# Kernel optimization log

Measured on AMD Instinct MI355X. Metric: run time of the kernel, lower is better.

## Reference

```python
import jax, jax.numpy as jnp
from jax import lax
import numpy as np

EPS = 1e-6
LN_EPS = 1e-3
B, T, F = 8, 2048, 80
STRIDE, NFILT = 2, 64
FEAT_P = 20              # ceil(80 / 4) after two stride-2 convs
CAPS_IN_N, CAPS_IN_D = 32, 8
CAPS_COV_N, CAPS_COV_D = 32, 8
CLASS_N, CAPS_CLS_D = 31, 8
WINDOW, LPAD, RPAD = 3, 1, 1
N_ITER = 3


def conv2d(x, w, b, stride):
    y = lax.conv_general_dilated(x, w, (stride, stride), 'SAME',
                                 dimension_numbers=('NHWC', 'HWIO', 'NHWC'))
    return y + b


def feat_mask(x, lengths, factor):
    # zero out time steps >= ceil(len/factor)
    S = x.shape[1]
    vl = jnp.ceil(lengths.astype(jnp.float32) / factor).astype(jnp.int32)
    m = (jnp.arange(S)[None, :] < vl[:, None]).astype(x.dtype)
    return x * m.reshape(m.shape + (1,) * (x.ndim - 2))


def squash(x, axis=-1):
    sq = jnp.sum(x * x, axis=axis, keepdims=True)
    return x * (sq / (1.0 + sq) / jnp.sqrt(sq + EPS))


def layernorm(x):
    mu = jnp.mean(x, -1, keepdims=True)
    var = jnp.var(x, -1, keepdims=True)
    return (x - mu) / jnp.sqrt(var + LN_EPS)


def window_concat(x):
    # [B,S,N,D] -> [B,S,N*WINDOW,D] (windowed context gather)
    S = x.shape[1]
    xp = jnp.pad(x, ((0, 0), (LPAD, RPAD), (0, 0), (0, 0)))
    return jnp.concatenate([xp[:, j:j + S] for j in range(WINDOW)], axis=2)


def dynamic_routing(u_hat, logit_mask):
    # u_hat: [B,S,I,O,D] -> v: [B,S,O,D]
    b0 = jnp.zeros(u_hat.shape[:4], u_hat.dtype)

    def body(b, _):
        c = jax.nn.softmax(b + logit_mask, axis=3)          # coupling coeffs
        s = jnp.einsum('bsio,bsiod->bsod', c, u_hat)
        v = squash(s, -1)
        b = b + jnp.einsum('bsiod,bsod->bsio', u_hat, v)    # agreement update
        return b, v

    _, vs = lax.scan(body, b0, None, length=N_ITER)
    return vs[-1]


def _forward(inputs, conv0_w1, conv0_b1, conv0_w2, conv0_b2,
             conv1_w1, conv1_b1, conv1_w2, conv1_b2,
             proj_w, proj_b, enc_w1, enc_b1, enc_w2, enc_b2,
             W0, B0, W1, B1, input_lengths):
    # --- CapsulationLayer: maxout conv feature extraction ---
    x = inputs[..., None]                                    # [B,T,F,1]
    x = jnp.maximum(conv2d(x, conv0_w1, conv0_b1, STRIDE),
                    conv2d(x, conv0_w2, conv0_b2, STRIDE))
    x = feat_mask(x, input_lengths, STRIDE)                  # [B,T/2,F/2,64]
    x = jnp.maximum(conv2d(x, conv1_w1, conv1_b1, STRIDE),
                    conv2d(x, conv1_w2, conv1_b2, STRIDE))
    x = feat_mask(x, input_lengths, STRIDE ** 2)             # [B,S,20,64]
    b, S = x.shape[0], x.shape[1]

    # --- primary capsules ---
    emb = x.reshape(b, S, FEAT_P * NFILT) @ proj_w + proj_b  # [B,S,32]
    emb = emb[..., None]                                     # [B,S,32,1]
    emb = jnp.maximum(conv2d(emb, enc_w1, enc_b1, 1),
                      conv2d(emb, enc_w2, enc_b2, 1))        # [B,S,32,8]
    emb = feat_mask(emb, input_lengths, STRIDE ** 2)
    emb = squash(emb, -1)
    emb = layernorm(emb.reshape(b, S, -1)).reshape(b, S, CAPS_IN_N, CAPS_IN_D)

    # --- caps layer 0: primary(windowed) -> convolution capsules ---
    win = window_concat(emb)                                 # [B,S,96,8]
    u = jnp.einsum('iodk,bsik->bsiod', W0, win) + B0[None, None]
    v = dynamic_routing(u, jnp.zeros((1, 1, 1, CAPS_COV_N), u.dtype))
    emb = layernorm(v.reshape(b, S, -1)).reshape(b, S, CAPS_COV_N, CAPS_COV_D)

    # --- caps layer 1: conv(windowed) -> class capsules (blank masked) ---
    win = window_concat(emb)                                 # [B,S,96,8]
    u = jnp.einsum('iodk,bsik->bsiod', W1, win) + B1[None, None]
    lm = jnp.concatenate([jnp.full((1, 1, 1, 1), -1e9, u.dtype),
                          jnp.zeros((1, 1, 1, CLASS_N - 1), u.dtype)], -1)
    v = dynamic_routing(u, lm)
    v = layernorm(v.reshape(b, S, -1)).reshape(b, S, CLASS_N, CAPS_CLS_D)

    # --- class capsule lengths + output layernorm ---
    out = jnp.sqrt(jnp.sum(v * v, -1) + EPS)                 # [B,S,31]
    return layernorm(out)


def setup_inputs() -> dict:
    key = jax.random.key(0)
    ks = list(jax.random.split(key, 24))
    n = lambda i, shape, s=0.1: jax.random.normal(ks[i], shape, jnp.float32) * s
    d = {
        'inputs': jax.random.normal(ks[0], (B, T, F), jnp.float32),
        'conv0_w1': n(1, (3, 3, 1, NFILT)), 'conv0_b1': n(2, (NFILT,)),
        'conv0_w2': n(3, (3, 3, 1, NFILT)), 'conv0_b2': n(4, (NFILT,)),
        'conv1_w1': n(5, (3, 3, NFILT, NFILT), 0.05), 'conv1_b1': n(6, (NFILT,)),
        'conv1_w2': n(7, (3, 3, NFILT, NFILT), 0.05), 'conv1_b2': n(8, (NFILT,)),
        'proj_w': n(9, (FEAT_P * NFILT, CAPS_IN_N), 0.02), 'proj_b': n(10, (CAPS_IN_N,)),
        'enc_w1': n(11, (3, 3, 1, CAPS_IN_D)), 'enc_b1': n(12, (CAPS_IN_D,)),
        'enc_w2': n(13, (3, 3, 1, CAPS_IN_D)), 'enc_b2': n(14, (CAPS_IN_D,)),
        'W0': n(15, (CAPS_IN_N * WINDOW, CAPS_COV_N, CAPS_COV_D, CAPS_IN_D)),
        'B0': n(16, (CAPS_IN_N * WINDOW, CAPS_COV_N, CAPS_COV_D)),
        'W1': n(17, (CAPS_COV_N * WINDOW, CLASS_N, CAPS_CLS_D, CAPS_COV_D)),
        'B1': n(18, (CAPS_COV_N * WINDOW, CLASS_N, CAPS_CLS_D)),
        'input_lengths': jax.random.randint(ks[19], (B,), T // 2, T + 1, jnp.int32),
    }
    return d


def reference(inputs, conv0_w1, conv0_b1, conv0_w2, conv0_b2,
              conv1_w1, conv1_b1, conv1_w2, conv1_b2,
              proj_w, proj_b, enc_w1, enc_b1, enc_w2, enc_b2,
              W0, B0, W1, B1, input_lengths):
    return _forward(inputs, conv0_w1, conv0_b1, conv0_w2, conv0_b2,
                    conv1_w1, conv1_b1, conv1_w2, conv1_b2,
                    proj_w, proj_b, enc_w1, enc_b1, enc_w2, enc_b2,
                    W0, B0, W1, B1, input_lengths)
```

## Files before the change

kernel.cpp:

```cpp
#include <hip/hip_runtime.h>

typedef unsigned short u16;
typedef unsigned int u32;
typedef short short8 __attribute__((ext_vector_type(8)));
typedef float f32x4 __attribute__((ext_vector_type(4)));
typedef _Float16 h2 __attribute__((ext_vector_type(2)));
typedef __fp16 fp16v2 __attribute__((ext_vector_type(2)));

#define DEV static __device__ __forceinline__

DEV float bf2f(u16 v) { return __uint_as_float((u32)v << 16); }
DEV u16 f2bf(float f) {
    u32 x = __float_as_uint(f);
    return (u16)((x + 0x7fffu + ((x >> 16) & 1u)) >> 16);
}
DEV u16 f2h(float f) {
    union { _Float16 h; u16 u; } c; c.h = (_Float16)f; return c.u;
}
DEV u32 pack2h(float a, float b) {
#if __has_builtin(__builtin_amdgcn_cvt_pkrtz)
    union { fp16v2 h; u32 u; } c;
    c.h = __builtin_amdgcn_cvt_pkrtz(a, b);
    return c.u;
#else
    union { u32 u; _Float16 h[2]; } c;
    c.h[0] = (_Float16)a; c.h[1] = (_Float16)b; return c.u;
#endif
}
DEV h2 u2h(u32 x) { union { u32 u; h2 h; } c; c.u = x; return c.h; }
DEV u32 h2u(h2 v) { union { h2 h; u32 u; } c; c.h = v; return c.u; }

#if __has_builtin(__builtin_amdgcn_fdot2)
DEV float dot2(u32 a, u32 b, float c) {
    return __builtin_amdgcn_fdot2(u2h(a), u2h(b), c, false);
}
#else
DEV float dot2(u32 a, u32 b, float c) {
    h2 ha = u2h(a), hb = u2h(b);
    c = fmaf((float)ha[0], (float)hb[0], c);
    return fmaf((float)ha[1], (float)hb[1], c);
}
#endif

constexpr int Bn = 8, Tn = 2048, Fn = 80, NF = 64;
constexpr int H1 = 1024, W1n = 40;
constexpr int Sn = 512,  W2n = 20;
constexpr int PK = 1280;
constexpr int I0 = 96;
constexpr int O0 = 32;
constexpr int O1 = 31;
constexpr int CPW = 52;
constexpr int NW0 = I0 * O0 * 8 * 8;
constexpr int NW1 = I0 * O1 * 8 * 8;
constexpr int KC1 = 576;

template <int CTRL>
DEV float dpp_mov(float x) {
    return __int_as_float(__builtin_amdgcn_update_dpp(
        0, __float_as_int(x), CTRL, 0xF, 0xF, true));
}
template <int CTRL>
DEV u32 dppu(u32 x) {
    return (u32)__builtin_amdgcn_update_dpp(0, (int)x, CTRL, 0xF, 0xF, true);
}
DEV float sum8(float x) {
    x += dpp_mov<0xB1>(x);
    x += dpp_mov<0x4E>(x);
    x += dpp_mov<0x141>(x);
    return x;
}
DEV u32 sum8h(u32 x) {
    x = h2u(u2h(x) + u2h(dppu<0xB1>(x)));
    x = h2u(u2h(x) + u2h(dppu<0x4E>(x)));
    x = h2u(u2h(x) + u2h(dppu<0x141>(x)));
    return x;
}

DEV float2 block_sum2(float a, float b, int tid, float* lds ) {
    #pragma unroll
    for (int m = 1; m < 64; m <<= 1) {
        a += __shfl_xor(a, m);
        b += __shfl_xor(b, m);
    }
    int wid = tid >> 6;
    __syncthreads();
    if ((tid & 63) == 0) { lds[wid * 2] = a; lds[wid * 2 + 1] = b; }
    __syncthreads();
    float ra = lds[0] + lds[2] + lds[4] + lds[6];
    float rb = lds[1] + lds[3] + lds[5] + lds[7];
    return make_float2(ra, rb);
}

__global__ void __launch_bounds__(256) k_prep(
        const float* __restrict__ w0, const float* __restrict__ w1c,
        const float* __restrict__ cw1, const float* __restrict__ cb1,
        const float* __restrict__ cw2, const float* __restrict__ cb2,
        u16* __restrict__ w0h, u16* __restrict__ w1h,
        u16* __restrict__ wt, float* __restrict__ biasi) {
    int idx = blockIdx.x * 256 + threadIdx.x;
    if (idx < NW0) w0h[idx] = f2h(w0[idx]);
    if (idx < NW1) w1h[idx] = f2h(w1c[idx]);
    if (idx < 128 * KC1) {
        int n = idx / KC1, k = idx - n * KC1;
        int c = n >> 1, s = n & 1;
        const float* w = s ? cw2 : cw1;
        wt[idx] = f2bf(w[k * 64 + c]);
    }
    if (idx < 128) {
        int c = idx >> 1, s = idx & 1;
        biasi[idx] = (s ? cb2 : cb1)[c];
    }
}

__global__ void __launch_bounds__(256) k_conv0(
        const float* __restrict__ in,
        const float* __restrict__ w1, const float* __restrict__ b1,
        const float* __restrict__ w2, const float* __restrict__ b2,
        const int* __restrict__ lens, u16* __restrict__ x1) {
    __shared__ float srow[3][82];
    int blk = blockIdx.x;
    int h = blk & (H1 - 1);
    int b = blk >> 10;
    int tid = threadIdx.x;

    for (int idx = tid; idx < 3 * 82; idx += 256) {
        int r = idx / 82, f = idx - r * 82;
        int t = 2 * h + r;
        float v = 0.f;
        if (t < Tn && f < Fn) v = in[(b * Tn + t) * Fn + f];
        srow[r][f] = v;
    }
    __syncthreads();

    int c = tid & 63;
    int wq = tid >> 6;
    float wr1[9], wr2[9];
    #pragma unroll
    for (int j = 0; j < 9; ++j) {
        wr1[j] = w1[j * 64 + c];
        wr2[j] = w2[j * 64 + c];
    }
    float bb1 = b1[c], bb2 = b2[c];
    int vl2 = (lens[b] + 1) >> 1;
    bool masked = (h >= vl2);

    u16* outbase = x1 + ((size_t)(b * H1 + h) * W1n) * 64 + c;
    #pragma unroll
    for (int p = 0; p < 10; ++p) {
        int w = wq * 10 + p;
        float a1 = bb1, a2 = bb2;
        #pragma unroll
        for (int r = 0; r < 3; ++r) {
            #pragma unroll
            for (int q = 0; q < 3; ++q) {
                float v = srow[r][2 * w + q];
                a1 = fmaf(v, wr1[r * 3 + q], a1);
                a2 = fmaf(v, wr2[r * 3 + q], a2);
            }
        }
        float out = masked ? 0.f : fmaxf(a1, a2);
        outbase[w * 64] = f2bf(out);
    }
}

__global__ void __launch_bounds__(256) k_conv1(
        const u16* __restrict__ x1, const u16* __restrict__ wt,
        const float* __restrict__ biasi, const int* __restrict__ lens,
        u16* __restrict__ x2) {
    constexpr int LD = 40;
    __shared__ u16 Al[2][128 * LD];
    __shared__ u16 Bl[2][128 * LD];
    __shared__ float bs_lds[128];

    int tid = threadIdx.x;
    int m0 = blockIdx.x * 128;
    int b = m0 / 10240;
    int vl4 = (lens[b] + 3) >> 2;

    if (tid < 128) bs_lds[tid] = biasi[tid];

    int srow = tid >> 1;
    int shalf = tid & 1;
    int am = m0 + srow;
    int aw = am % 20;
    int ah = (am / 20) % 512;
    const u16* abase = x1 + (((size_t)b * 1024 + 2 * ah) * 40 + 2 * aw) * 64;
    const u16* bbase = wt + srow * KC1;

    const uint4 uz = make_uint4(0, 0, 0, 0);
    uint4 na0, na1, nb0, nb1;
    {
        const u16* ap = abase + shalf * 16;
        na0 = *(const uint4*)(ap);
        na1 = *(const uint4*)(ap + 8);
        const u16* bp = bbase + shalf * 16;
        nb0 = *(const uint4*)(bp);
        nb1 = *(const uint4*)(bp + 8);
    }
    {
        u16* awp = &Al[0][srow * LD + shalf * 16];
        *(uint4*)awp = na0; *(uint4*)(awp + 8) = na1;
        u16* bwp = &Bl[0][srow * LD + shalf * 16];
        *(uint4*)bwp = nb0; *(uint4*)(bwp + 8) = nb1;
    }
    __syncthreads();

    int lane = tid & 63;
    int wid = tid >> 6;
    int mw = wid & 1, nw = wid >> 1;
    int frow = lane & 15;
    int koff = (lane >> 4) * 8;

    f32x4 acc[4][4] = {};
    int buf = 0;

    #pragma unroll
    for (int kc = 0; kc < 18; ++kc) {
        if (kc < 17) {
            int kn = kc + 1;
            int rq = kn >> 1, ci0 = (kn & 1) * 32;
            int r = rq / 3, q = rq - 3 * r;
            bool v = (2 * ah + r < 1024) && (2 * aw + q < 40);
            const u16* ap = abase + (r * 40 + q) * 64 + ci0 + shalf * 16;
            na0 = v ? *(const uint4*)(ap) : uz;
            na1 = v ? *(const uint4*)(ap + 8) : uz;
            const u16* bp = bbase + kn * 32 + shalf * 16;
            nb0 = *(const uint4*)(bp);
            nb1 = *(const uint4*)(bp + 8);
        }
        const u16* Ar = &Al[buf][(mw * 64 + frow) * LD + koff];
        const u16* Br = &Bl[buf][(nw * 64 + frow) * LD + koff];
        short8 af[4], bfr[4];
        #pragma unroll
        for (int s = 0; s < 4; ++s) {
            af[s]  = *(const short8*)(Ar + s * 16 * LD);
            bfr[s] = *(const short8*)(Br + s * 16 * LD);
        }
        #pragma unroll
        for (int sm = 0; sm < 4; ++sm)
            #pragma unroll
            for (int sn = 0; sn < 4; ++sn)
                acc[sm][sn] = __builtin_amdgcn_mfma_f32_16x16x32_bf16(
                    af[sm], bfr[sn], acc[sm][sn], 0, 0, 0);
        if (kc < 17) {
            buf ^= 1;
            u16* awp = &Al[buf][srow * LD + shalf * 16];
            *(uint4*)awp = na0; *(uint4*)(awp + 8) = na1;
            u16* bwp = &Bl[buf][srow * LD + shalf * 16];
            *(uint4*)bwp = nb0; *(uint4*)(bwp + 8) = nb1;
            __syncthreads();
        }
    }

    int orow = (lane >> 4) * 4;
    int ncol = lane & 15;
    #pragma unroll
    for (int sm = 0; sm < 4; ++sm) {
        #pragma unroll
        for (int sn = 0; sn < 4; ++sn) {
            int np = nw * 64 + sn * 16 + ncol;
            float bia = bs_lds[np];
            #pragma unroll
            for (int r = 0; r < 4; ++r) {
                float v = acc[sm][sn][r] + bia;
                float o = fmaxf(v, dpp_mov<0xB1>(v));
                if (!(lane & 1)) {
                    int gm = m0 + mw * 64 + sm * 16 + orow + r;
                    int w = gm % 20;
                    int h = (gm / 20) % 512;
                    float res = (h >= vl4) ? 0.f : o;
                    x2[((size_t)(b * 512 + h) * 20 + w) * 64 + (np >> 1)] = f2bf(res);
                }
            }
        }
    }
}

__global__ void __launch_bounds__(256) k_proj(
        const u16* __restrict__ x2, const float* __restrict__ pw,
        const float* __restrict__ pb, float* __restrict__ proj) {
    int bs = blockIdx.x;
    int tid = threadIdx.x;
    int o = tid & 31, part = tid >> 5;
    const u16* row = &x2[(size_t)bs * PK];
    float acc = 0.f;
    int k0 = part * 160;
    #pragma unroll 8
    for (int k = 0; k < 160; ++k)
        acc = fmaf(bf2f(row[k0 + k]), pw[(k0 + k) * 32 + o], acc);
    __shared__ float red[256];
    red[tid] = acc;
    __syncthreads();
    if (tid < 32) {
        float s = 0.f;
        #pragma unroll
        for (int p = 0; p < 8; ++p) s += red[p * 32 + tid];
        proj[bs * 32 + tid] = s + pb[tid];
    }
}

__global__ void __launch_bounds__(256) k_enc(
        const float* __restrict__ proj,
        const float* __restrict__ ew1, const float* __restrict__ eb1,
        const float* __restrict__ ew2, const float* __restrict__ eb2,
        const int* __restrict__ lens, float* __restrict__ emb0) {
    int bs = blockIdx.x;
    int s = bs & (Sn - 1);
    int b = bs >> 9;
    int tid = threadIdx.x;
    __shared__ float rows[3][32];
    __shared__ float red[8];
    if (tid < 96) {
        int r = tid >> 5, n = tid & 31;
        int sr = s - 1 + r;
        rows[r][n] = (sr >= 0 && sr < Sn) ? proj[(b * Sn + sr) * 32 + n] : 0.f;
    }
    __syncthreads();

    int n = tid >> 3, d = tid & 7;
    float a1 = eb1[d], a2 = eb2[d];
    #pragma unroll
    for (int r = 0; r < 3; ++r) {
        #pragma unroll
        for (int q = 0; q < 3; ++q) {
            int nn = n - 1 + q;
            if (nn >= 0 && nn < 32) {
                float v = rows[r][nn];
                int wi = (r * 3 + q) * 8 + d;
                a1 = fmaf(v, ew1[wi], a1);
                a2 = fmaf(v, ew2[wi], a2);
            }
        }
    }
    float x = fmaxf(a1, a2);
    int vl4 = (lens[b] + 3) >> 2;
    if (s >= vl4) x = 0.f;

    float sq = sum8(x * x);
    x = x * (sq / (1.f + sq) * rsqrtf(sq + 1e-6f));

    float2 ss = block_sum2(x, x * x, tid, red);
    float mu = ss.x * (1.f / 256.f);
    float var = ss.y * (1.f / 256.f) - mu * mu;
    emb0[bs * 256 + tid] = (x - mu) * rsqrtf(var + 1e-3f);
}

__global__ void __launch_bounds__(256, 3) k_caps0(
        const float* __restrict__ embin, const u16* __restrict__ W0,
        const float* __restrict__ B0, float* __restrict__ embout) {
    int pb2 = blockIdx.x;
    int b = pb2 >> 8;
    int s0 = (pb2 & 255) << 1;
    int tid = threadIdx.x;
    int o = tid >> 3;

    __shared__ __align__(16) u32 win2[2][I0 * 4];
    __shared__ float blog[2][I0 * 33];
    __shared__ __align__(16) u32 cpk[2][O0 * CPW];
    __shared__ float red[8];
    u16* cph0 = (u16*)cpk[0];
    u16* cph1 = (u16*)cpk[1];

    for (int idx = tid; idx < 2 * I0 * 4; idx += 256) {
        int g = idx >= I0 * 4;
        int lidx = idx - g * I0 * 4;
        int i = lidx >> 2, kk = lidx & 3;
        int sr = s0 + g + (i >> 5) - 1;
        float a = 0.f, bv = 0.f;
        if (sr >= 0 && sr < Sn) {
            const float* p = &embin[(b * Sn + sr) * 256 + (i & 31) * 8 + kk * 2];
            a = p[0]; bv = p[1];
        }
        win2[g][lidx] = pack2h(a, bv);
    }
    for (int i = tid; i < 2 * I0 * 33; i += 256) blog[0][i] = 0.f;
    __syncthreads();

    u32 u_pk0[48], u_pk1[48];
    {
        const uint4* Wv = (const uint4*)W0;
        const uint4* wl0 = (const uint4*)win2[0];
        const uint4* wl1 = (const uint4*)win2[1];
        #pragma unroll
        for (int ii = 0; ii < 48; ++ii) {
            int i0 = 2 * ii, i1 = 2 * ii + 1;
            uint4 wv0 = Wv[i0 * 256 + tid];
            uint4 wv1 = Wv[i1 * 256 + tid];
            float bb0 = B0[i0 * 256 + tid];
            float bb1 = B0[i1 * 256 + tid];
            uint4 wa0 = wl0[i0], wa1 = wl0[i1];
            float a0 = bb0, a1 = bb1;
            a0 = dot2(wv0.x, wa0.x, a0);
            a0 = dot2(wv0.y, wa0.y, a0);
            a0 = dot2(wv0.z, wa0.z, a0);
            a0 = dot2(wv0.w, wa0.w, a0);
            a1 = dot2(wv1.x, wa1.x, a1);
            a1 = dot2(wv1.y, wa1.y, a1);
            a1 = dot2(wv1.z, wa1.z, a1);
            a1 = dot2(wv1.w, wa1.w, a1);
            u_pk0[ii] = pack2h(a0, a1);
            uint4 wb0 = wl1[i0], wb1 = wl1[i1];
            a0 = bb0; a1 = bb1;
            a0 = dot2(wv0.x, wb0.x, a0);
            a0 = dot2(wv0.y, wb0.y, a0);
            a0 = dot2(wv0.z, wb0.z, a0);
            a0 = dot2(wv0.w, wb0.w, a0);
            a1 = dot2(wv1.x, wb1.x, a1);
            a1 = dot2(wv1.y, wb1.y, a1);
            a1 = dot2(wv1.z, wb1.z, a1);
            a1 = dot2(wv1.w, wb1.w, a1);
            u_pk1[ii] = pack2h(a0, a1);
        }
    }

    float vv0 = 0.f, vv1 = 0.f;
    for (int it = 0; it < 3; ++it) {
        if (tid < 192) {
            int i = tid >> 1, hf = tid & 1;
            int o0 = hf * 16;
            #pragma unroll
            for (int g = 0; g < 2; ++g) {
                float ex[16];
                float ssum = 0.f;
                #pragma unroll
                for (int j = 0; j < 16; ++j) {
                    ex[j] = __expf(blog[g][i * 33 + o0 + j]);
                    ssum += ex[j];
                }
                ssum += dpp_mov<0xB1>(ssum);
                float inv = __builtin_amdgcn_rcpf(ssum);
                u16* cc = g ? cph1 : cph0;
                #pragma unroll
                for (int j = 0; j < 16; ++j)
                    cc[(o0 + j) * (CPW * 2) + i] = f2h(ex[j] * inv);
            }
        }
        __syncthreads();
        {
            float sv0 = 0.f, sv1 = 0.f;
            const uint4* cr0 = (const uint4*)&cpk[0][o * CPW];
            const uint4* cr1 = (const uint4*)&cpk[1][o * CPW];
            #pragma unroll
            for (int q4 = 0; q4 < 12; ++q4) {
                uint4 c0 = cr0[q4], c1 = cr1[q4];
                sv0 = dot2(u_pk0[q4 * 4 + 0], c0.x, sv0);
                sv0 = dot2(u_pk0[q4 * 4 + 1], c0.y, sv0);
                sv0 = dot2(u_pk0[q4 * 4 + 2], c0.z, sv0);
                sv0 = dot2(u_pk0[q4 * 4 + 3], c0.w, sv0);
                sv1 = dot2(u_pk1[q4 * 4 + 0], c1.x, sv1);
                sv1 = dot2(u_pk1[q4 * 4 + 1], c1.y, sv1);
                sv1 = dot2(u_pk1[q4 * 4 + 2], c1.z, sv1);
                sv1 = dot2(u_pk1[q4 * 4 + 3], c1.w, sv1);
            }
            float sq0 = sum8(sv0 * sv0);
            float sq1 = sum8(sv1 * sv1);
            vv0 = sv0 * (sq0 / (1.f + sq0) * rsqrtf(sq0 + 1e-6f));
            vv1 = sv1 * (sq1 / (1.f + sq1) * rsqrtf(sq1 + 1e-6f));
        }
        if (it < 2) {
            u32 va = pack2h(vv0, vv0), vb = pack2h(vv1, vv1);
            #pragma unroll
            for (int ii = 0; ii < 48; ++ii) {
                u32 p0 = sum8h(h2u(u2h(u_pk0[ii]) * u2h(va)));
                u32 p1 = sum8h(h2u(u2h(u_pk1[ii]) * u2h(vb)));
                if ((tid & 7) == 0) {
                    h2 q0 = u2h(p0), q1 = u2h(p1);
                    blog[0][(2 * ii) * 33 + o]     += (float)q0[0];
                    blog[0][(2 * ii + 1) * 33 + o] += (float)q0[1];
                    blog[1][(2 * ii) * 33 + o]     += (float)q1[0];
                    blog[1][(2 * ii + 1) * 33 + o] += (float)q1[1];
                }
            }
            __syncthreads();
        }
    }

    float2 ss = block_sum2(vv0, vv0 * vv0, tid, red);
    float mu = ss.x * (1.f / 256.f);
    float var = ss.y * (1.f / 256.f) - mu * mu;
    embout[(b * Sn + s0) * 256 + tid] = (vv0 - mu) * rsqrtf(var + 1e-3f);
    ss = block_sum2(vv1, vv1 * vv1, tid, red);
    mu = ss.x * (1.f / 256.f);
    var = ss.y * (1.f / 256.f) - mu * mu;
    embout[(b * Sn + s0 + 1) * 256 + tid] = (vv1 - mu) * rsqrtf(var + 1e-3f);
}

__global__ void __launch_bounds__(256, 3) k_caps1(
        const float* __restrict__ embin, const u16* __restrict__ W1,
        const float* __restrict__ B1, float* __restrict__ outp) {
    int pb2 = blockIdx.x;
    int b = pb2 >> 8;
    int s0 = (pb2 & 255) << 1;
    int tid = threadIdx.x;
    int o = tid >> 3, d = tid & 7;
    bool valid = (o < O1);
    int oc = valid ? o : (O1 - 1);
    int ocd = oc * 8 + d;

    __shared__ __align__(16) u32 win2[2][I0 * 4];
    __shared__ float blog[2][I0 * 33];
    __shared__ __align__(16) u32 cpk[2][O1 * CPW];
    __shared__ float red[8];
    __shared__ float lenb[2][O1];
    __shared__ float mv2[4];
    u16* cph0 = (u16*)cpk[0];
    u16* cph1 = (u16*)cpk[1];

    for (int idx = tid; idx < 2 * I0 * 4; idx += 256) {
        int g = idx >= I0 * 4;
        int lidx = idx - g * I0 * 4;
        int i = lidx >> 2, kk = lidx & 3;
        int sr = s0 + g + (i >> 5) - 1;
        float a = 0.f, bv = 0.f;
        if (sr >= 0 && sr < Sn) {
            const float* p = &embin[(b * Sn + sr) * 256 + (i & 31) * 8 + kk * 2];
            a = p[0]; bv = p[1];
        }
        win2[g][lidx] = pack2h(a, bv);
    }
    for (int i = tid; i < 2 * I0 * 33; i += 256) blog[0][i] = 0.f;
    for (int i = tid; i < CPW; i += 256) { cpk[0][i] = 0; cpk[1][i] = 0; }
    __syncthreads();

    u32 u_pk0[48], u_pk1[48];
    {
        const uint4* Wv = (const uint4*)W1;
        const uint4* wl0 = (const uint4*)win2[0];
        const uint4* wl1 = (const uint4*)win2[1];
        #pragma unroll
        for (int ii = 0; ii < 48; ++ii) {
            int i0 = 2 * ii, i1 = 2 * ii + 1;
            uint4 wv0 = Wv[i0 * 248 + ocd];
            uint4 wv1 = Wv[i1 * 248 + ocd];
            float bb0 = B1[i0 * 248 + ocd];
            float bb1 = B1[i1 * 248 + ocd];
            uint4 wa0 = wl0[i0], wa1 = wl0[i1];
            float a0 = bb0, a1 = bb1;
            a0 = dot2(wv0.x, wa0.x, a0);
            a0 = dot2(wv0.y, wa0.y, a0);
            a0 = dot2(wv0.z, wa0.z, a0);
            a0 = dot2(wv0.w, wa0.w, a0);
            a1 = dot2(wv1.x, wa1.x, a1);
            a1 = dot2(wv1.y, wa1.y, a1);
            a1 = dot2(wv1.z, wa1.z, a1);
            a1 = dot2(wv1.w, wa1.w, a1);
            u_pk0[ii] = pack2h(a0, a1);
            uint4 wb0 = wl1[i0], wb1 = wl1[i1];
            a0 = bb0; a1 = bb1;
            a0 = dot2(wv0.x, wb0.x, a0);
            a0 = dot2(wv0.y, wb0.y, a0);
            a0 = dot2(wv0.z, wb0.z, a0);
            a0 = dot2(wv0.w, wb0.w, a0);
            a1 = dot2(wv1.x, wb1.x, a1);
            a1 = dot2(wv1.y, wb1.y, a1);
            a1 = dot2(wv1.z, wb1.z, a1);
            a1 = dot2(wv1.w, wb1.w, a1);
            u_pk1[ii] = pack2h(a0, a1);
        }
    }

    float vv0 = 0.f, vv1 = 0.f;
    for (int it = 0; it < 3; ++it) {
        if (tid < 192) {
            int i = tid >> 1, hf = tid & 1;
            int lo = hf ? 16 : 1;
            #pragma unroll
            for (int g = 0; g < 2; ++g) {
                float ex[15];
                float ssum = 0.f;
                #pragma unroll
                for (int j = 0; j < 15; ++j) {
                    ex[j] = __expf(blog[g][i * 33 + lo + j]);
                    ssum += ex[j];
                }
                ssum += dpp_mov<0xB1>(ssum);
                float inv = __builtin_amdgcn_rcpf(ssum);
                u16* cc = g ? cph1 : cph0;
                #pragma unroll
                for (int j = 0; j < 15; ++j)
                    cc[(lo + j) * (CPW * 2) + i] = f2h(ex[j] * inv);
            }
        }
        __syncthreads();
        {
            float sv0 = 0.f, sv1 = 0.f;
            const uint4* cr0 = (const uint4*)&cpk[0][oc * CPW];
            const uint4* cr1 = (const uint4*)&cpk[1][oc * CPW];
            #pragma unroll
            for (int q4 = 0; q4 < 12; ++q4) {
                uint4 c0 = cr0[q4], c1 = cr1[q4];
                sv0 = dot2(u_pk0[q4 * 4 + 0], c0.x, sv0);
                sv0 = dot2(u_pk0[q4 * 4 + 1], c0.y, sv0);
                sv0 = dot2(u_pk0[q4 * 4 + 2], c0.z, sv0);
                sv0 = dot2(u_pk0[q4 * 4 + 3], c0.w, sv0);
                sv1 = dot2(u_pk1[q4 * 4 + 0], c1.x, sv1);
                sv1 = dot2(u_pk1[q4 * 4 + 1], c1.y, sv1);
                sv1 = dot2(u_pk1[q4 * 4 + 2], c1.z, sv1);
                sv1 = dot2(u_pk1[q4 * 4 + 3], c1.w, sv1);
            }
            float sq0 = sum8(sv0 * sv0);
            float sq1 = sum8(sv1 * sv1);
            vv0 = sv0 * (sq0 / (1.f + sq0) * rsqrtf(sq0 + 1e-6f));
            vv1 = sv1 * (sq1 / (1.f + sq1) * rsqrtf(sq1 + 1e-6f));
            if (!valid) { vv0 = 0.f; vv1 = 0.f; }
        }
        if (it < 2) {
            u32 va = pack2h(vv0, vv0), vb = pack2h(vv1, vv1);
            #pragma unroll
            for (int ii = 0; ii < 48; ++ii) {
                u32 p0 = sum8h(h2u(u2h(u_pk0[ii]) * u2h(va)));
                u32 p1 = sum8h(h2u(u2h(u_pk1[ii]) * u2h(vb)));
                if ((tid & 7) == 0 && valid) {
                    h2 q0 = u2h(p0), q1 = u2h(p1);
                    blog[0][(2 * ii) * 33 + o]     += (float)q0[0];
                    blog[0][(2 * ii + 1) * 33 + o] += (float)q0[1];
                    blog[1][(2 * ii) * 33 + o]     += (float)q1[0];
                    blog[1][(2 * ii + 1) * 33 + o] += (float)q1[1];
                }
            }
            __syncthreads();
        }
    }

    float2 ss = block_sum2(vv0, vv0 * vv0, tid, red);
    float mu = ss.x * (1.f / 248.f);
    float var = ss.y * (1.f / 248.f) - mu * mu;
    float y0 = (vv0 - mu) * rsqrtf(var + 1e-3f);
    ss = block_sum2(vv1, vv1 * vv1, tid, red);
    mu = ss.x * (1.f / 248.f);
    var = ss.y * (1.f / 248.f) - mu * mu;
    float y1 = (vv1 - mu) * rsqrtf(var + 1e-3f);

    float sq0 = sum8(y0 * y0);
    float sq1 = sum8(y1 * y1);
    if (valid && (tid & 7) == 0) {
        lenb[0][o] = sqrtf(sq0 + 1e-6f);
        lenb[1][o] = sqrtf(sq1 + 1e-6f);
    }
    __syncthreads();

    if (tid < 2) {
        float s1 = 0.f, s2 = 0.f;
        for (int oo = 0; oo < O1; ++oo) { float t = lenb[tid][oo]; s1 += t; s2 += t * t; }
        float m2 = s1 / 31.f;
        mv2[tid * 2] = m2;
        mv2[tid * 2 + 1] = rsqrtf(s2 / 31.f - m2 * m2 + 1e-3f);
    }
    __syncthreads();
    if (tid < O1) {
        outp[(size_t)(b * Sn + s0) * O1 + tid] = (lenb[0][tid] - mv2[0]) * mv2[1];
        outp[(size_t)(b * Sn + s0 + 1) * O1 + tid] = (lenb[1][tid] - mv2[2]) * mv2[3];
    }
}

extern "C" void kernel_launch(void* const* d_in, const int* in_sizes, int n_in,
                              void* d_out, int out_size, void* d_ws, size_t ws_size,
                              hipStream_t stream) {
    const float* inputs = (const float*)d_in[0];
    const float* c0w1 = (const float*)d_in[1];
    const float* c0b1 = (const float*)d_in[2];
    const float* c0w2 = (const float*)d_in[3];
    const float* c0b2 = (const float*)d_in[4];
    const float* c1w1 = (const float*)d_in[5];
    const float* c1b1 = (const float*)d_in[6];
    const float* c1w2 = (const float*)d_in[7];
    const float* c1b2 = (const float*)d_in[8];
    const float* pw   = (const float*)d_in[9];
    const float* pb   = (const float*)d_in[10];
    const float* ew1  = (const float*)d_in[11];
    const float* eb1  = (const float*)d_in[12];
    const float* ew2  = (const float*)d_in[13];
    const float* eb2  = (const float*)d_in[14];
    const float* W0   = (const float*)d_in[15];
    const float* B0   = (const float*)d_in[16];
    const float* W1   = (const float*)d_in[17];
    const float* B1   = (const float*)d_in[18];
    const int* lens = (const int*)d_in[19];

    char* ws = (char*)d_ws;
    u16*   x1    = (u16*)(ws);
    u16*   x2    = (u16*)(ws + 41943040);
    float* proj  = (float*)(ws + 52428800);
    float* emb0  = (float*)(ws + 52953088);
    float* emb1  = (float*)(ws + 57147392);
    u16*   W0h   = (u16*)(ws + 61341696);
    u16*   W1h   = (u16*)(ws + 61734912);
    u16*   wt    = (u16*)(ws + 62115840);
    float* biasi = (float*)(ws + 62263296);

    k_prep<<<(NW0 + 255) / 256, 256, 0, stream>>>(
        W0, W1, c1w1, c1b1, c1w2, c1b2, W0h, W1h, wt, biasi);
    k_conv0<<<Bn * H1, 256, 0, stream>>>(
        inputs, c0w1, c0b1, c0w2, c0b2, lens, x1);
    k_conv1<<<640, 256, 0, stream>>>(x1, wt, biasi, lens, x2);
    k_proj<<<Bn * Sn, 256, 0, stream>>>(x2, pw, pb, proj);
    k_enc<<<Bn * Sn, 256, 0, stream>>>(proj, ew1, eb1, ew2, eb2, lens, emb0);
    k_caps0<<<Bn * Sn / 2, 256, 0, stream>>>(emb0, W0h, B0, emb1);
    k_caps1<<<Bn * Sn / 2, 256, 0, stream>>>(emb1, W1h, B1, (float*)d_out);
}
```

Measured before the change: 353.7 us.

## Shrink routing LDS footprint with packed fp16 logits and aliased buffers

Routing logits are now stored as packed fp16 pairs rather than fp32. The input window buffer is aliased with the coupling-coefficient buffer, and a barrier is added so the reuse is safe. The coefficient writes are merged into full 32-bit stores using a DPP lane swap, and launch bounds rise from 3 to 6 blocks per SM. The goal is to cut LDS usage so more blocks stay resident, at the cost of fp16 accumulation error in the logits and tighter register limits that could cause spills.

After: 511.7 us. +44.7%, slower.

```diff
diff --git a/kernel.cpp b/kernel.cpp
--- a/kernel.cpp
+++ b/kernel.cpp
@@ -16,6 +16,9 @@
 }
 DEV u16 f2h(float f) {
     union { _Float16 h; u16 u; } c; c.h = (_Float16)f; return c.u;
+}
+DEV float h16f(u16 v) {
+    union { u16 u; _Float16 h; } c; c.u = v; return (float)c.h;
 }
 DEV u32 pack2h(float a, float b) {
 #if __has_builtin(__builtin_amdgcn_cvt_pkrtz)
@@ -345,7 +348,7 @@
     emb0[bs * 256 + tid] = (x - mu) * rsqrtf(var + 1e-3f);
 }
 
-__global__ void __launch_bounds__(256, 3) k_caps0(
+__global__ void __launch_bounds__(256, 6) k_caps0(
         const float* __restrict__ embin, const u16* __restrict__ W0,
         const float* __restrict__ B0, float* __restrict__ embout) {
     int pb2 = blockIdx.x;
@@ -354,12 +357,10 @@
     int tid = threadIdx.x;
     int o = tid >> 3;
 
-    __shared__ __align__(16) u32 win2[2][I0 * 4];
-    __shared__ float blog[2][I0 * 33];
-    __shared__ __align__(16) u32 cpk[2][O0 * CPW];
+    constexpr int CR = O0 * CPW;
+    __shared__ __align__(16) u32 shbuf[2][CR];
+    __shared__ u32 blgp[2][48 * 33];
     __shared__ float red[8];
-    u16* cph0 = (u16*)cpk[0];
-    u16* cph1 = (u16*)cpk[1];
 
     for (int idx = tid; idx < 2 * I0 * 4; idx += 256) {
         int g = idx >= I0 * 4;
@@ -371,16 +372,16 @@
             const float* p = &embin[(b * Sn + sr) * 256 + (i & 31) * 8 + kk * 2];
             a = p[0]; bv = p[1];
         }
-        win2[g][lidx] = pack2h(a, bv);
-    }
-    for (int i = tid; i < 2 * I0 * 33; i += 256) blog[0][i] = 0.f;
+        shbuf[g][lidx] = pack2h(a, bv);
+    }
+    for (int idx = tid; idx < 2 * 48 * 33; idx += 256) ((u32*)blgp)[idx] = 0;
     __syncthreads();
 
     u32 u_pk0[48], u_pk1[48];
     {
         const uint4* Wv = (const uint4*)W0;
-        const uint4* wl0 = (const uint4*)win2[0];
-        const uint4* wl1 = (const uint4*)win2[1];
+        const uint4* wl0 = (const uint4*)shbuf[0];
+        const uint4* wl1 = (const uint4*)shbuf[1];
         #pragma unroll
         for (int ii = 0; ii < 48; ++ii) {
             int i0 = 2 * ii, i1 = 2 * ii + 1;
@@ -412,34 +413,42 @@
             u_pk1[ii] = pack2h(a0, a1);
         }
     }
+    __syncthreads();
 
     float vv0 = 0.f, vv1 = 0.f;
     for (int it = 0; it < 3; ++it) {
         if (tid < 192) {
             int i = tid >> 1, hf = tid & 1;
+            int sh = (i & 1) * 16;
+            int ip = i >> 1;
             int o0 = hf * 16;
             #pragma unroll
             for (int g = 0; g < 2; ++g) {
+                const u32* brow = &blgp[g][ip * 33];
                 float ex[16];
                 float ssum = 0.f;
                 #pragma unroll
                 for (int j = 0; j < 16; ++j) {
-                    ex[j] = __expf(blog[g][i * 33 + o0 + j]);
+                    ex[j] = __expf(h16f((u16)(brow[o0 + j] >> sh)));
                     ssum += ex[j];
                 }
                 ssum += dpp_mov<0xB1>(ssum);
                 float inv = __builtin_amdgcn_rcpf(ssum);
-                u16* cc = g ? cph1 : cph0;
+                u32* crow = shbuf[g];
                 #pragma unroll
-                for (int j = 0; j < 16; ++j)
-                    cc[(o0 + j) * (CPW * 2) + i] = f2h(ex[j] * inv);
+                for (int j = 0; j < 16; ++j) {
+                    u32 mine = f2h(ex[j] * inv);
+                    u32 part = dppu<0x4E>(mine);
+                    if (!(tid & 2))
+                        crow[(o0 + j) * CPW + ip] = mine | (part << 16);
+                }
             }
         }
         __syncthreads();
         {
             float sv0 = 0.f, sv1 = 0.f;
-            const uint4* cr0 = (const uint4*)&cpk[0][o * CPW];
-            const uint4* cr1 = (const uint4*)&cpk[1][o * CPW];
+            const uint4* cr0 = (const uint4*)&shbuf[0][o * CPW];
+            const uint4* cr1 = (const uint4*)&shbuf[1][o * CPW];
             #pragma unroll
             for (int q4 = 0; q4 < 12; ++q4) {
                 uint4 c0 = cr0[q4], c1 = cr1[q4];
@@ -464,11 +473,9 @@
                 u32 p0 = sum8h(h2u(u2h(u_pk0[ii]) * u2h(va)));
                 u32 p1 = sum8h(h2u(u2h(u_pk1[ii]) * u2h(vb)));
                 if ((tid & 7) == 0) {
-                    h2 q0 = u2h(p0), q1 = u2h(p1);
-                    blog[0][(2 * ii) * 33 + o]     += (float)q0[0];
-                    blog[0][(2 * ii + 1) * 33 + o] += (float)q0[1];
-                    blog[1][(2 * ii) * 33 + o]     += (float)q1[0];
-                    blog[1][(2 * ii + 1) * 33 + o] += (float)q1[1];
+                    int idx = ii * 33 + o;
+                    blgp[0][idx] = h2u(u2h(blgp[0][idx]) + u2h(p0));
+                    blgp[1][idx] = h2u(u2h(blgp[1][idx]) + u2h(p1));
                 }
             }
             __syncthreads();
@@ -485,7 +492,7 @@
     embout[(b * Sn + s0 + 1) * 256 + tid] = (vv1 - mu) * rsqrtf(var + 1e-3f);
 }
 
-__global__ void __launch_bounds__(256, 3) k_caps1(
+__global__ void __launch_bounds__(256, 6) k_caps1(
         const float* __restrict__ embin, const u16* __restrict__ W1,
         const float* __restrict__ B1, float* __restrict__ outp) {
     int pb2 = blockIdx.x;
@@ -497,14 +504,12 @@
     int oc = valid ? o : (O1 - 1);
     int ocd = oc * 8 + d;
 
-    __shared__ __align__(16) u32 win2[2][I0 * 4];
-    __shared__ float blog[2][I0 * 33];
-    __shared__ __align__(16) u32 cpk[2][O1 * CPW];
+    constexpr int CR = O1 * CPW;
+    __shared__ __align__(16) u32 shbuf[2][CR];
+    __shared__ u32 blgp[2][48 * 33];
     __shared__ float red[8];
     __shared__ float lenb[2][O1];
     __shared__ float mv2[4];
-    u16* cph0 = (u16*)cpk[0];
-    u16* cph1 = (u16*)cpk[1];
 
     for (int idx = tid; idx < 2 * I0 * 4; idx += 256) {
         int g = idx >= I0 * 4;
@@ -516,17 +521,16 @@
             const float* p = &embin[(b * Sn + sr) * 256 + (i & 31) * 8 + kk * 2];
             a = p[0]; bv = p[1];
         }
-        win2[g][lidx] = pack2h(a, bv);
-    }
-    for (int i = tid; i < 2 * I0 * 33; i += 256) blog[0][i] = 0.f;
-    for (int i = tid; i < CPW; i += 256) { cpk[0][i] = 0; cpk[1][i] = 0; }
+        shbuf[g][lidx] = pack2h(a, bv);
+    }
+    for (int idx = tid; idx < 2 * 48 * 33; idx += 256) ((u32*)blgp)[idx] = 0;
     __syncthreads();
 
     u32 u_pk0[48], u_pk1[48];
     {
         const uint4* Wv = (const uint4*)W1;
-        const uint4* wl0 = (const uint4*)win2[0];
-        const uint4* wl1 = (const uint4*)win2[1];
+        const uint4* wl0 = (const uint4*)shbuf[0];
+        const uint4* wl1 = (const uint4*)shbuf[1];
         #pragma unroll
         for (int ii = 0; ii < 48; ++ii) {
             int i0 = 2 * ii, i1 = 2 * ii + 1;
@@ -558,34 +562,45 @@
             u_pk1[ii] = pack2h(a0, a1);
         }
     }
+    __syncthreads();
 
     float vv0 = 0.f, vv1 = 0.f;
     for (int it = 0; it < 3; ++it) {
         if (tid < 192) {
             int i = tid >> 1, hf = tid & 1;
+            int sh = (i & 1) * 16;
+            int ip = i >> 1;
             int lo = hf ? 16 : 1;
             #pragma unroll
             for (int g = 0; g < 2; ++g) {
+                const u32* brow = &blgp[g][ip * 33];
                 float ex[15];
                 float ssum = 0.f;
                 #pragma unroll
                 for (int j = 0; j < 15; ++j) {
-                    ex[j] = __expf(blog[g][i * 33 + lo + j]);
+                    ex[j] = __expf(h16f((u16)(brow[lo + j] >> sh)));
                     ssum += ex[j];
                 }
                 ssum += dpp_mov<0xB1>(ssum);
                 float inv = __builtin_amdgcn_rcpf(ssum);
-                u16* cc = g ? cph1 : cph0;
+                u32* crow = shbuf[g];
                 #pragma unroll
-                for (int j = 0; j < 15; ++j)
-                    cc[(lo + j) * (CPW * 2) + i] = f2h(ex[j] * inv);
-            }
+                for (int j = 0; j < 15; ++j) {
+                    u32 mine = f2h(ex[j] * inv);
+                    u32 part = dppu<0x4E>(mine);
+                    if (!(tid & 2))
+                        crow[(lo + j) * CPW + ip] = mine | (part << 16);
+                }
+            }
+        } else {
+            int z = tid - 192;
+            if (z < CPW) { shbuf[0][z] = 0; shbuf[1][z] = 0; }
         }
         __syncthreads();
         {
             float sv0 = 0.f, sv1 = 0.f;
-            const uint4* cr0 = (const uint4*)&cpk[0][oc * CPW];
-            const uint4* cr1 = (const uint4*)&cpk[1][oc * CPW];
+            const uint4* cr0 = (const uint4*)&shbuf[0][oc * CPW];
+            const uint4* cr1 = (const uint4*)&shbuf[1][oc * CPW];
             #pragma unroll
             for (int q4 = 0; q4 < 12; ++q4) {
                 uint4 c0 = cr0[q4], c1 = cr1[q4];
@@ -611,11 +626,9 @@
                 u32 p0 = sum8h(h2u(u2h(u_pk0[ii]) * u2h(va)));
                 u32 p1 = sum8h(h2u(u2h(u_pk1[ii]) * u2h(vb)));
                 if ((tid & 7) == 0 && valid) {
-                    h2 q0 = u2h(p0), q1 = u2h(p1);
-                    blog[0][(2 * ii) * 33 + o]     += (float)q0[0];
-                    blog[0][(2 * ii + 1) * 33 + o] += (float)q0[1];
-                    blog[1][(2 * ii) * 33 + o]     += (float)q1[0];
-                    blog[1][(2 * ii + 1) * 33 + o] += (float)q1[1];
+                    int idx = ii * 33 + o;
+                    blgp[0][idx] = h2u(u2h(blgp[0][idx]) + u2h(p0));
+                    blgp[1][idx] = h2u(u2h(blgp[1][idx]) + u2h(p1));
                 }
             }
             __syncthreads();
```
